# Optimization experiments

Hardware: AMD Instinct MI355X
Metric: run time of the kernel (lower is better)

The kernel has to match this reference:

```python
import jax, jax.numpy as jnp
import numpy as np

B, T, D = 2, 2048, 1024
NH, NKV, HD = 16, 4, 64
BASE, TSL, QGI = 10000.0, 1024, 1.5
EPS = 1.1920929e-07  # torch.finfo(float32).eps used by F.rms_norm default


def _rope_cos_sin(seq_len, rd):
    # Rotary.forward with self.rd == head_dim (Attn sets rd=0 -> full rotation)
    if seq_len > TSL:  # NTK-style base rescale branch
        nb = BASE * (seq_len / TSL) ** (rd / (rd - 2))
    else:
        nb = BASE
    inv = 1.0 / nb ** (jnp.arange(0, rd, 2, dtype=jnp.float32) / rd)
    fr = jnp.arange(seq_len, dtype=jnp.float32)[:, None] * inv[None, :]
    return jnp.cos(fr)[None, :, None, :], jnp.sin(fr)[None, :, None, :]


def _apply_rope(x, cos, sin):
    h = x.shape[-1] // 2
    x1, x2 = x[..., :h], x[..., h:]
    return jnp.concatenate([x1 * cos + x2 * sin, -x1 * sin + x2 * cos], axis=-1)


def _rms_norm(x):
    return x * jax.lax.rsqrt(jnp.mean(x * x, axis=-1, keepdims=True) + EPS)


def setup_inputs() -> dict:
    key = jax.random.key(0)
    ks = jax.random.split(key, 8)
    s = jnp.float32(0.02)
    return {
        "x": jax.random.normal(ks[0], (B, T, D), jnp.float32),
        "qw": jax.random.normal(ks[1], (NH * HD, D), jnp.float32) * s,
        "kw": jax.random.normal(ks[2], (NKV * HD, D), jnp.float32) * s,
        "vw": jax.random.normal(ks[3], (NKV * HD, D), jnp.float32) * s,
        "ow": jax.random.normal(ks[4], (D, D), jnp.float32) * s,
        "ve": jax.random.normal(ks[5], (B, T, NKV * HD), jnp.float32) * s,
        "v0": jax.random.normal(ks[6], (B, T, NKV, HD), jnp.float32) * s,
        "q_gain": jnp.full((NH,), QGI, jnp.float32),
        "vr_lambda": jnp.array([0.5, 0.5], jnp.float32),
        "gate_w": jnp.zeros((NH, D), jnp.float32),      # nn.init.zeros_
        "gate_b": jnp.full((NH,), 4.0, jnp.float32),    # nn.init.constant_(4.0)
    }


def reference(x, qw, kw, vw, ow, ve, v0, q_gain, vr_lambda, gate_w, gate_b):
    # projections
    q = (x @ qw.T).reshape(B, T, NH, HD)
    k = (x @ kw.T).reshape(B, T, NKV, HD)
    v = (x @ vw.T + ve).reshape(B, T, NKV, HD)
    raw_v = v  # returned when vr=True
    v = vr_lambda[0] * v0 + vr_lambda[1] * v  # value residual
    # qk rms-norm + rope (full head dim since self.rd == 0) + per-head q gain
    q = _rms_norm(q)
    k = _rms_norm(k)
    cos, sin = _rope_cos_sin(T, HD)
    q = _apply_rope(q, cos, sin)
    k = _apply_rope(k, cos, sin)
    q = q * q_gain[None, None, :, None]
    # causal GQA attention (nh query heads share nkv kv heads)
    G = NH // NKV
    qg = q.reshape(B, T, NKV, G, HD)
    scale = 1.0 / np.sqrt(HD).astype(np.float32)
    scores = jnp.einsum('bqhgd,bkhd->bhgqk', qg, k) * scale  # [B,NKV,G,T,T]
    causal = jnp.tril(jnp.ones((T, T), bool))
    scores = jnp.where(causal[None, None, None], scores, jnp.finfo(scores.dtype).min)
    p = jax.nn.softmax(scores, axis=-1)
    y = jnp.einsum('bhgqk,bkhd->bqhgd', p, v).reshape(B, T, NH, HD)
    # gated attention output
    gate = jax.nn.sigmoid(x @ gate_w.T + gate_b)  # [B,T,NH]
    y = y * gate[..., None]
    out = y.reshape(B, T, D) @ ow.T
    return out, raw_v
```

## Files before the change

### kernel.cpp

```cpp
#include <hip/hip_runtime.h>
#include <math.h>

#define BB 2
#define TT 2048
#define DD 1024
#define NH 16
#define NKV 4
#define HD 64
#define EPSF 1.1920929e-07f
#define LOG2_NB 14.319970444065578
#define SCALE_LOG2E 0.18033688011112042f
#define FIXMAX 17.5f

typedef __attribute__((ext_vector_type(8))) short bf16x8;
typedef __attribute__((ext_vector_type(4))) float f32x4;

__device__ inline short f2bf(float f) {
    unsigned u = __builtin_bit_cast(unsigned, f);
    unsigned r = (u + 0x7fffu + ((u >> 16) & 1u)) >> 16;
    return (short)r;
}
__device__ inline unsigned cvt_pk_bf16(float a, float b) {
    unsigned r;
    asm("v_cvt_pk_bf16_f32 %0, %1, %2" : "=v"(r) : "v"(a), "v"(b));
    return r;
}

#define GSTAGE(buf, k0, Abase, Bbase)                                                   \
{                                                                                       \
    _Pragma("unroll")                                                                   \
    for (int i_ = 0; i_ < 2; i_++) {                                                    \
        int off = w*2048 + i_*1024;                      \
        int g = (off >> 4) + lane;                                   \
        int row = g >> 2, c = g & 3;                                                    \
        int cg = c ^ (row & 3);                                        \
        const short* ga = (Abase) + (size_t)(m0 + row)*1024 + (k0) + cg*8;              \
        __builtin_amdgcn_global_load_lds(                                               \
            (const __attribute__((address_space(1))) void*)ga,                          \
            (__attribute__((address_space(3))) void*)((char*)&As[buf][0] + off), 16, 0, 0); \
        const short* gb = (Bbase) + (size_t)(n0 + row)*1024 + (k0) + cg*8;              \
        __builtin_amdgcn_global_load_lds(                                               \
            (const __attribute__((address_space(1))) void*)gb,                          \
            (__attribute__((address_space(3))) void*)((char*)&Bs[buf][0] + off), 16, 0, 0); \
    }                                                                                   \
}

#define GEMM_MAIN_LOOP(kbeg, kend, Abase, Bbase)                                        \
    GSTAGE(0, (kbeg), (Abase), (Bbase));                                                \
    __syncthreads();                                                                    \
    for (int k0 = (kbeg); k0 < (kend); k0 += 32) {                                      \
        int cur = ((k0 - (kbeg)) >> 5) & 1;                                             \
        bf16x8 af[4], bfr[4];                                                           \
        _Pragma("unroll")                                                               \
        for (int tm = 0; tm < 4; tm++) {                                                \
            int row = wy*64 + tm*16 + lc;                                               \
            af[tm] = *(const bf16x8*)(&As[cur][0] + row*32 + ((quad*8) ^ ((row&3)*8))); \
        }                                                                               \
        _Pragma("unroll")                                                               \
        for (int tn = 0; tn < 4; tn++) {                                                \
            int row = wx*64 + tn*16 + lc;                                               \
            bfr[tn] = *(const bf16x8*)(&Bs[cur][0] + row*32 + ((quad*8) ^ ((row&3)*8))); \
        }                                                                               \
        if (k0 + 32 < (kend)) GSTAGE(cur ^ 1, k0 + 32, (Abase), (Bbase));               \
        _Pragma("unroll")                                                               \
        for (int tm = 0; tm < 4; tm++)                                                  \
            _Pragma("unroll")                                                           \
            for (int tn = 0; tn < 4; tn++)                                              \
                acc[tm][tn] = __builtin_amdgcn_mfma_f32_16x16x32_bf16(af[tm], bfr[tn], acc[tm][tn], 0, 0, 0); \
        __syncthreads();                                                                \
    }

__global__ __launch_bounds__(256, 2) void gemm_qkv_fused(
    const float* __restrict__ x, const float* __restrict__ qw,
    const float* __restrict__ kw, const float* __restrict__ vw,
    const float* __restrict__ gw, const float* __restrict__ ow,
    const float* __restrict__ ve, const float* __restrict__ v0,
    const float* __restrict__ q_gain, const float* __restrict__ vr_lambda,
    const float* __restrict__ gb_, float* __restrict__ gate,
    short* __restrict__ qbh, short* __restrict__ kbh, short* __restrict__ vtb,
    float* __restrict__ rawv, short* __restrict__ ow16)
{
    __shared__ short As[2][128*32];
    __shared__ short Bs[2][128*32];
    int tid = threadIdx.x;
    int w = tid >> 6, lane = tid & 63;
    int quad = lane >> 4, lc = lane & 15;
    int wy = w >> 1, wx = w & 1;
    int m0 = blockIdx.y * 128, n0 = blockIdx.x * 128;

    int g0 = w*128 + lane;
    int g1 = w*128 + 64 + lane;
    int rA0 = g0 >> 2, rA1 = g1 >> 2;
    int cg0 = (g0 & 3) ^ (rA0 & 3);
    int cg1 = (g1 & 3) ^ (rA1 & 3);
    const float* aptr0 = x + (size_t)(m0 + rA0)*1024 + cg0*8;
    const float* aptr1 = x + (size_t)(m0 + rA1)*1024 + cg1*8;
    int nB0 = n0 + rA0, nB1 = n0 + rA1;
    const float* bptr0;
    if      (nB0 < 1024) bptr0 = qw + (size_t)nB0*1024;
    else if (nB0 < 1280) bptr0 = kw + (size_t)(nB0-1024)*1024;
    else if (nB0 < 1536) bptr0 = vw + (size_t)(nB0-1280)*1024;
    else                 bptr0 = gw + (size_t)((nB0-1536)&15)*1024;
    const float* bptr1;
    if      (nB1 < 1024) bptr1 = qw + (size_t)nB1*1024;
    else if (nB1 < 1280) bptr1 = kw + (size_t)(nB1-1024)*1024;
    else if (nB1 < 1536) bptr1 = vw + (size_t)(nB1-1280)*1024;
    else                 bptr1 = gw + (size_t)((nB1-1536)&15)*1024;
    bptr0 += cg0*8; bptr1 += cg1*8;
    unsigned bmask0 = (nB0 < 1552) ? 0xFFFFFFFFu : 0u;
    unsigned bmask1 = (nB1 < 1552) ? 0xFFFFFFFFu : 0u;

    float4 A0a, A0b, A1a, A1b, B0a, B0b, B1a, B1b;

    #define QSTG_LOAD(k0)                                                   \
    {                                                                       \
        A0a = *(const float4*)(aptr0 + (k0));                               \
        A0b = *(const float4*)(aptr0 + (k0) + 4);                           \
        A1a = *(const float4*)(aptr1 + (k0));                               \
        A1b = *(const float4*)(aptr1 + (k0) + 4);                           \
        B0a = *(const float4*)(bptr0 + (k0));                               \
        B0b = *(const float4*)(bptr0 + (k0) + 4);                           \
        B1a = *(const float4*)(bptr1 + (k0));                               \
        B1b = *(const float4*)(bptr1 + (k0) + 4);                           \
    }

    #define QSTG_WRITE(buf)                                                 \
    {                                                                       \
        unsigned q0, q1, q2, q3; int4 pk;                                   \
        q0 = cvt_pk_bf16(A0a.x, A0a.y); q1 = cvt_pk_bf16(A0a.z, A0a.w);     \
        q2 = cvt_pk_bf16(A0b.x, A0b.y); q3 = cvt_pk_bf16(A0b.z, A0b.w);     \
        pk = (int4){(int)q0,(int)q1,(int)q2,(int)q3};                       \
        *(int4*)((char*)&As[buf][0] + w*2048 + lane*16) = pk;               \
        q0 = cvt_pk_bf16(A1a.x, A1a.y); q1 = cvt_pk_bf16(A1a.z, A1a.w);     \
        q2 = cvt_pk_bf16(A1b.x, A1b.y); q3 = cvt_pk_bf16(A1b.z, A1b.w);     \
        pk = (int4){(int)q0,(int)q1,(int)q2,(int)q3};                       \
        *(int4*)((char*)&As[buf][0] + w*2048 + 1024 + lane*16) = pk;        \
        q0 = cvt_pk_bf16(B0a.x, B0a.y) & bmask0;                            \
        q1 = cvt_pk_bf16(B0a.z, B0a.w) & bmask0;                            \
        q2 = cvt_pk_bf16(B0b.x, B0b.y) & bmask0;                            \
        q3 = cvt_pk_bf16(B0b.z, B0b.w) & bmask0;                            \
        pk = (int4){(int)q0,(int)q1,(int)q2,(int)q3};                       \
        *(int4*)((char*)&Bs[buf][0] + w*2048 + lane*16) = pk;               \
        q0 = cvt_pk_bf16(B1a.x, B1a.y) & bmask1;                            \
        q1 = cvt_pk_bf16(B1a.z, B1a.w) & bmask1;                            \
        q2 = cvt_pk_bf16(B1b.x, B1b.y) & bmask1;                            \
        q3 = cvt_pk_bf16(B1b.z, B1b.w) & bmask1;                            \
        pk = (int4){(int)q0,(int)q1,(int)q2,(int)q3};                       \
        *(int4*)((char*)&Bs[buf][0] + w*2048 + 1024 + lane*16) = pk;        \
    }

    f32x4 acc[4][4];
    #pragma unroll
    for (int i = 0; i < 4; i++)
        #pragma unroll
        for (int j = 0; j < 4; j++) acc[i][j] = (f32x4){0.f,0.f,0.f,0.f};

    QSTG_LOAD(0);
    QSTG_WRITE(0);
    __syncthreads();

    for (int k0 = 0; k0 < 1024; k0 += 32) {
        int cur = (k0 >> 5) & 1;
        bool pre = (k0 + 32) < 1024;
        bf16x8 af[4], bfr[4];
        #pragma unroll
        for (int tm = 0; tm < 4; tm++) {
            int row = wy*64 + tm*16 + lc;
            af[tm] = *(const bf16x8*)(&As[cur][0] + row*32 + ((quad*8) ^ ((row&3)*8)));
        }
        #pragma unroll
        for (int tn = 0; tn < 4; tn++) {
            int row = wx*64 + tn*16 + lc;
            bfr[tn] = *(const bf16x8*)(&Bs[cur][0] + row*32 + ((quad*8) ^ ((row&3)*8)));
        }
        if (pre) QSTG_LOAD(k0 + 32);
        #pragma unroll
        for (int tm = 0; tm < 4; tm++)
            #pragma unroll
            for (int tn = 0; tn < 4; tn++)
                acc[tm][tn] = __builtin_amdgcn_mfma_f32_16x16x32_bf16(af[tm], bfr[tn], acc[tm][tn], 0, 0, 0);
        if (pre) QSTG_WRITE(cur ^ 1);
        __syncthreads();
    }

    int hc = n0 + wx*64;
    if (hc < 1280) {
        bool isq = (hc < 1024);
        int h = isq ? (hc >> 6) : ((hc - 1024) >> 6);
        float gsc = isq ? (q_gain[h] * SCALE_LOG2E) : 1.0f;
        short* dst = isq ? qbh : kbh;
        int nhh = isq ? 16 : 4;
        float inv0 = (float)exp2((double)lc * (-LOG2_NB / 32.0));
        float inv1 = (float)exp2((double)(lc + 16) * (-LOG2_NB / 32.0));
        #pragma unroll
        for (int tm = 0; tm < 4; tm++) {
            #pragma unroll
            for (int r = 0; r < 4; r++) {
                int m = m0 + wy*64 + tm*16 + quad*4 + r;
                int b = m >> 11, t = m & (TT - 1);
                float a0 = acc[tm][0][r], a1 = acc[tm][1][r];
                float a2 = acc[tm][2][r], a3 = acc[tm][3][r];
                float ss = a0*a0 + a1*a1 + a2*a2 + a3*a3;
                ss += __shfl_xor(ss, 1);
                ss += __shfl_xor(ss, 2);
                ss += __shfl_xor(ss, 4);
                ss += __shfl_xor(ss, 8);
                float rn = rsqrtf(ss * (1.0f/64.0f) + EPSF);
                a0 *= rn; a1 *= rn; a2 *= rn; a3 *= rn;
                float sn0, cs0, sn1, cs1;
                sincosf((float)t * inv0, &sn0, &cs0);
                sincosf((float)t * inv1, &sn1, &cs1);
                float o0 = a0*cs0 + a2*sn0;
                float o1 = a1*cs1 + a3*sn1;
                float o2 = a2*cs0 - a0*sn0;
                float o3 = a3*cs1 - a1*sn1;
                size_t base = (((size_t)(b*nhh + h))*2048 + t)*64 + lc;
                dst[base +  0] = f2bf(o0 * gsc);
                dst[base + 16] = f2bf(o1 * gsc);
                dst[base + 32] = f2bf(o2 * gsc);
                dst[base + 48] = f2bf(o3 * gsc);
            }
        }
    } else if (hc < 1536) {
        int kvh = (hc - 1280) >> 6;
        float l0 = vr_lambda[0], l1 = vr_lambda[1];
        short* lbase = (w < 2) ? &As[w][0] : &Bs[w - 2][0];
        #pragma unroll
        for (int tm = 0; tm < 4; tm++) {
            #pragma unroll
            for (int r = 0; r < 4; r++) {
                int m = m0 + wy*64 + tm*16 + quad*4 + r;
                int tl = tm*16 + quad*4 + r;
                size_t off = (size_t)m*256 + kvh*64 + lc;
                #pragma unroll
                for (int tn = 0; tn < 4; tn++) {
                    int d = tn*16 + lc;
                    float val = acc[tm][tn][r] + ve[off + tn*16];
                    rawv[off + tn*16] = val;
                    lbase[d*64 + (tl ^ ((d & 7) * 8))] = f2bf(l0 * v0[off + tn*16] + l1 * val);
                }
            }
        }
        int b = m0 >> 11;
        int t0g = (m0 & 2047) + wy*64;
        short* vdst = vtb + (size_t)(b*4 + kvh)*64*2048;
        #pragma unroll
        for (int j = 0; j < 16; j++) {
            int d = quad + j*4;
            int tc = lc*4;
            short4 vv = *(const short4*)&lbase[d*64 + (tc ^ ((d & 7) * 8))];
            *(short4*)&vdst[(size_t)d*2048 + t0g + tc] = vv;
        }
    } else if (hc == 1536) {
        #pragma unroll
        for (int tm = 0; tm < 4; tm++)
            #pragma unroll
            for (int r = 0; r < 4; r++) {
                int m = m0 + wy*64 + tm*16 + quad*4 + r;
                float lg = acc[tm][0][r] + gb_[lc];
                gate[(size_t)m*16 + lc] = 1.0f / (1.0f + __expf(-lg));
            }
    }

    int gtid = (blockIdx.y * 13 + blockIdx.x) * 256 + tid;
    for (int idx = gtid; idx < 262144; idx += 106496) {
        float4 v = ((const float4*)ow)[idx];
        short4 o;
        o.x = f2bf(v.x); o.y = f2bf(v.y); o.z = f2bf(v.z); o.w = f2bf(v.w);
        ((short4*)ow16)[idx] = o;
    }
    #undef QSTG_LOAD
    #undef QSTG_WRITE
}

__global__ __launch_bounds__(256, 4) void gemm_mfma(
    const short* __restrict__ A, const short* __restrict__ Bmat,
    float* __restrict__ C, int ldc, int klen)
{
    __shared__ short As[2][128*32];
    __shared__ short Bs[2][128*32];
    int tid = threadIdx.x;
    int w = tid >> 6, lane = tid & 63;
    int quad = lane >> 4, lc = lane & 15;
    int wy = w >> 1, wx = w & 1;
    int m0 = blockIdx.y * 128, n0 = blockIdx.x * 128;

    f32x4 acc[4][4];
    #pragma unroll
    for (int i = 0; i < 4; i++)
        #pragma unroll
        for (int j = 0; j < 4; j++) acc[i][j] = (f32x4){0.f,0.f,0.f,0.f};

    GEMM_MAIN_LOOP(0, klen, A, Bmat);

    #pragma unroll
    for (int tm = 0; tm < 4; tm++)
        #pragma unroll
        for (int r = 0; r < 4; r++) {
            int m = m0 + wy*64 + tm*16 + quad*4 + r;
            #pragma unroll
            for (int tn = 0; tn < 4; tn++) {
                int n = n0 + wx*64 + tn*16 + lc;
                C[(size_t)m*ldc + n] = acc[tm][tn][r];
            }
        }
}

__global__ __launch_bounds__(256, 4) void flash_mfma(
    const short* __restrict__ qbh, const short* __restrict__ kbh,
    const short* __restrict__ vtb, const float* __restrict__ gate,
    short* __restrict__ y16)
{
    __shared__ short Ks[2][64*64];
    __shared__ short Vt[2][64*64];
    __shared__ short Ps[4][16*64];

    int bh = blockIdx.x;
    int b = bh >> 4, h = bh & 15, kvh = h >> 2;
    int qt = 31 - blockIdx.y;
    int tid = threadIdx.x;
    int w = tid >> 6, lane = tid & 63;
    int quad = lane >> 4, lc = lane & 15;

    const short* qbase = qbh + (((size_t)bh)*2048 + qt*64 + w*16 + lc)*64;
    bf16x8 qf0 = *(const bf16x8*)(qbase + quad*8);
    bf16x8 qf1 = *(const bf16x8*)(qbase + 32 + quad*8);

    f32x4 o[4];
    #pragma unroll
    for (int i = 0; i < 4; i++) o[i] = (f32x4){0.f,0.f,0.f,0.f};
    f32x4 l4 = (f32x4){0.f,0.f,0.f,0.f};
    const bf16x8 ones = {(short)0x3F80,(short)0x3F80,(short)0x3F80,(short)0x3F80,
                         (short)0x3F80,(short)0x3F80,(short)0x3F80,(short)0x3F80};

    const size_t kbase = ((size_t)(b*4 + kvh))*2048*64;
    const size_t vbase = ((size_t)(b*4 + kvh))*64*2048;

    #define STAGE(buf, kt)                                                              \
    {                                                                                   \
        _Pragma("unroll")                                                               \
        for (int i = 0; i < 2; i++) {                                                   \
            int off = w*2048 + i*1024;                                                  \
            int g = (off >> 4) + lane;                                                  \
            int row = g >> 3, c = g & 7;                                                \
            int cg = c ^ (row & 7);                                                     \
            const short* gk = kbh + kbase + (size_t)((kt)*64 + row)*64 + cg*8;          \
            __builtin_amdgcn_global_load_lds(                                           \
                (const __attribute__((address_space(1))) void*)gk,                      \
                (__attribute__((address_space(3))) void*)((char*)Ks[buf] + off), 16, 0, 0); \
            const short* gv = vtb + vbase + (size_t)row*2048 + (kt)*64 + cg*8;          \
            __builtin_amdgcn_global_load_lds(                                           \
                (const __attribute__((address_space(1))) void*)gv,                      \
                (__attribute__((address_space(3))) void*)((char*)Vt[buf] + off), 16, 0, 0); \
        }                                                                               \
    }

    STAGE(0, 0);
    __syncthreads();

    short* ps = Ps[w];

    for (int kt = 0; kt <= qt; kt++) {
        int cur = kt & 1;
        bool diag = (kt == qt);

        bf16x8 kf0[4], kf1[4], vf0[4], vf1[4];
        #pragma unroll
        for (int kn = 0; kn < 4; kn++) {
            int row = kn*16 + lc;
            int sw = (row & 7) * 8;
            const short* kr = Ks[cur] + row*64;
            kf0[kn] = *(const bf16x8*)(kr + ((quad*8) ^ sw));
            kf1[kn] = *(const bf16x8*)(kr + ((quad*8 + 32) ^ sw));
            const short* vr = Vt[cur] + row*64;
            vf0[kn] = *(const bf16x8*)(vr + ((quad*8) ^ sw));
            vf1[kn] = *(const bf16x8*)(vr + ((quad*8 + 32) ^ sw));
        }
        if (kt < qt) STAGE(cur ^ 1, kt + 1);

        f32x4 s4[4];
        #pragma unroll
        for (int kn = 0; kn < 4; kn++) {
            f32x4 acc = (f32x4){0.f,0.f,0.f,0.f};
            acc = __builtin_amdgcn_mfma_f32_16x16x32_bf16(kf0[kn], qf0, acc, 0, 0, 0);
            acc = __builtin_amdgcn_mfma_f32_16x16x32_bf16(kf1[kn], qf1, acc, 0, 0, 0);
            s4[kn] = acc;
        }

        #pragma unroll
        for (int kn = 0; kn < 4; kn++) {
            float p0 = __builtin_amdgcn_exp2f(s4[kn][0] - FIXMAX);
            float p1 = __builtin_amdgcn_exp2f(s4[kn][1] - FIXMAX);
            float p2 = __builtin_amdgcn_exp2f(s4[kn][2] - FIXMAX);
            float p3 = __builtin_amdgcn_exp2f(s4[kn][3] - FIXMAX);
            if (diag) {
                int keyb = kn*16 + quad*4, qv = w*16 + lc;
                if (keyb + 0 > qv) p0 = 0.f;
                if (keyb + 1 > qv) p1 = 0.f;
                if (keyb + 2 > qv) p2 = 0.f;
                if (keyb + 3 > qv) p3 = 0.f;
            }
            int c = kn*4 + quad;
            int cs = c ^ ((lc & 7) << 1);
            int2 pk;
            pk.x = (int)cvt_pk_bf16(p0, p1);
            pk.y = (int)cvt_pk_bf16(p2, p3);
            *(int2*)(ps + lc*64 + cs*4) = pk;
        }
        __asm__ volatile("s_waitcnt lgkmcnt(0)" ::: "memory");
        int u0 = (0*4 + quad) ^ (lc & 7);
        int u1 = (1*4 + quad) ^ (lc & 7);
        bf16x8 pf0 = *(const bf16x8*)(ps + lc*64 + u0*8);
        bf16x8 pf1 = *(const bf16x8*)(ps + lc*64 + u1*8);

        #pragma unroll
        for (int dn = 0; dn < 4; dn++) {
            o[dn] = __builtin_amdgcn_mfma_f32_16x16x32_bf16(pf0, vf0[dn], o[dn], 0, 0, 0);
            o[dn] = __builtin_amdgcn_mfma_f32_16x16x32_bf16(pf1, vf1[dn], o[dn], 0, 0, 0);
        }
        l4 = __builtin_amdgcn_mfma_f32_16x16x32_bf16(pf0, ones, l4, 0, 0, 0);
        l4 = __builtin_amdgcn_mfma_f32_16x16x32_bf16(pf1, ones, l4, 0, 0, 0);
        __syncthreads();
    }

    #pragma unroll
    for (int r = 0; r < 4; r++) {
        int row = b*2048 + qt*64 + w*16 + quad*4 + r;
        float g = gate[(size_t)row*16 + h] / l4[r];
        #pragma unroll
        for (int dn = 0; dn < 4; dn++)
            y16[(size_t)row*1024 + h*64 + dn*16 + lc] = f2bf(o[dn][r] * g);
    }
}

extern "C" void kernel_launch(void* const* d_in, const int* in_sizes, int n_in,
                              void* d_out, int out_size, void* d_ws, size_t ws_size,
                              hipStream_t stream) {
    (void)in_sizes; (void)n_in; (void)out_size; (void)ws_size;
    const float* x  = (const float*)d_in[0];
    const float* qw = (const float*)d_in[1];
    const float* kw = (const float*)d_in[2];
    const float* vw = (const float*)d_in[3];
    const float* ow = (const float*)d_in[4];
    const float* ve = (const float*)d_in[5];
    const float* v0 = (const float*)d_in[6];
    const float* qg = (const float*)d_in[7];
    const float* vl = (const float*)d_in[8];
    const float* gw = (const float*)d_in[9];
    const float* gb = (const float*)d_in[10];

    float* out  = (float*)d_out;
    float* rawv = out + (size_t)BB*TT*DD;

    float* p    = (float*)d_ws;
    short* ow16 = (short*)p;        p += 524288;
    short* qbh  = (short*)p;        p += 2097152;
    short* kbh  = (short*)p;        p += 524288;
    short* vtb  = (short*)p;        p += 524288;
    float* gt   = p;                p += 65536;
    short* y16  = (short*)p;

    gemm_qkv_fused<<<dim3(13, 32), 256, 0, stream>>>(x, qw, kw, vw, gw, ow,
                                                     ve, v0, qg, vl, gb, gt,
                                                     qbh, kbh, vtb, rawv, ow16);
    flash_mfma<<<dim3(32, 32), 256, 0, stream>>>(qbh, kbh, vtb, gt, y16);
    gemm_mfma<<<dim3(8, 32), 256, 0, stream>>>(y16, ow16, out, 1024, 1024);
}
```

Before: 184.5 us.

## Deepen QKV GEMM global prefetch to two stages and swap grid block order

The fused QKV projection GEMM now keeps two register-staged global loads in flight, unrolling the k loop by two so the next-next tile's fp32 loads are issued while the current tile is being multiplied. The grid is also transposed so consecutive blocks share the same weight column tile and walk over rows of x, which changes L2 reuse of the weight matrices. The deeper prefetch doubles the staging registers, which could raise register pressure under the two-blocks-per-CU launch bound and risk spills.

```diff
diff --git a/kernel.cpp b/kernel.cpp
--- a/kernel.cpp
+++ b/kernel.cpp
@@ -86,7 +86,7 @@
     int w = tid >> 6, lane = tid & 63;
     int quad = lane >> 4, lc = lane & 15;
     int wy = w >> 1, wx = w & 1;
-    int m0 = blockIdx.y * 128, n0 = blockIdx.x * 128;
+    int m0 = blockIdx.x * 128, n0 = blockIdx.y * 128;
 
     int g0 = w*128 + lane;
     int g1 = w*128 + 64 + lane;
@@ -110,44 +110,64 @@
     unsigned bmask0 = (nB0 < 1552) ? 0xFFFFFFFFu : 0u;
     unsigned bmask1 = (nB1 < 1552) ? 0xFFFFFFFFu : 0u;
 
-    float4 A0a, A0b, A1a, A1b, B0a, B0b, B1a, B1b;
-
-    #define QSTG_LOAD(k0)                                                   \
+    float4 A0a0,A0b0,A1a0,A1b0,B0a0,B0b0,B1a0,B1b0;
+    float4 A0a1,A0b1,A1a1,A1b1,B0a1,B0b1,B1a1,B1b1;
+
+    #define QSTG_LOAD(S, k0)                                                \
     {                                                                       \
-        A0a = *(const float4*)(aptr0 + (k0));                               \
-        A0b = *(const float4*)(aptr0 + (k0) + 4);                           \
-        A1a = *(const float4*)(aptr1 + (k0));                               \
-        A1b = *(const float4*)(aptr1 + (k0) + 4);                           \
-        B0a = *(const float4*)(bptr0 + (k0));                               \
-        B0b = *(const float4*)(bptr0 + (k0) + 4);                           \
-        B1a = *(const float4*)(bptr1 + (k0));                               \
-        B1b = *(const float4*)(bptr1 + (k0) + 4);                           \
-    }
-
-    #define QSTG_WRITE(buf)                                                 \
+        A0a##S = *(const float4*)(aptr0 + (k0));                            \
+        A0b##S = *(const float4*)(aptr0 + (k0) + 4);                        \
+        A1a##S = *(const float4*)(aptr1 + (k0));                            \
+        A1b##S = *(const float4*)(aptr1 + (k0) + 4);                        \
+        B0a##S = *(const float4*)(bptr0 + (k0));                            \
+        B0b##S = *(const float4*)(bptr0 + (k0) + 4);                        \
+        B1a##S = *(const float4*)(bptr1 + (k0));                            \
+        B1b##S = *(const float4*)(bptr1 + (k0) + 4);                        \
+    }
+
+    #define QSTG_WRITE(S, buf)                                              \
     {                                                                       \
         unsigned q0, q1, q2, q3; int4 pk;                                   \
-        q0 = cvt_pk_bf16(A0a.x, A0a.y); q1 = cvt_pk_bf16(A0a.z, A0a.w);     \
-        q2 = cvt_pk_bf16(A0b.x, A0b.y); q3 = cvt_pk_bf16(A0b.z, A0b.w);     \
+        q0 = cvt_pk_bf16(A0a##S.x, A0a##S.y); q1 = cvt_pk_bf16(A0a##S.z, A0a##S.w); \
+        q2 = cvt_pk_bf16(A0b##S.x, A0b##S.y); q3 = cvt_pk_bf16(A0b##S.z, A0b##S.w); \
         pk = (int4){(int)q0,(int)q1,(int)q2,(int)q3};                       \
         *(int4*)((char*)&As[buf][0] + w*2048 + lane*16) = pk;               \
-        q0 = cvt_pk_bf16(A1a.x, A1a.y); q1 = cvt_pk_bf16(A1a.z, A1a.w);     \
-        q2 = cvt_pk_bf16(A1b.x, A1b.y); q3 = cvt_pk_bf16(A1b.z, A1b.w);     \
+        q0 = cvt_pk_bf16(A1a##S.x, A1a##S.y); q1 = cvt_pk_bf16(A1a##S.z, A1a##S.w); \
+        q2 = cvt_pk_bf16(A1b##S.x, A1b##S.y); q3 = cvt_pk_bf16(A1b##S.z, A1b##S.w); \
         pk = (int4){(int)q0,(int)q1,(int)q2,(int)q3};                       \
         *(int4*)((char*)&As[buf][0] + w*2048 + 1024 + lane*16) = pk;        \
-        q0 = cvt_pk_bf16(B0a.x, B0a.y) & bmask0;                            \
-        q1 = cvt_pk_bf16(B0a.z, B0a.w) & bmask0;                            \
-        q2 = cvt_pk_bf16(B0b.x, B0b.y) & bmask0;                            \
-        q3 = cvt_pk_bf16(B0b.z, B0b.w) & bmask0;                            \
+        q0 = cvt_pk_bf16(B0a##S.x, B0a##S.y) & bmask0;                      \
+        q1 = cvt_pk_bf16(B0a##S.z, B0a##S.w) & bmask0;                      \
+        q2 = cvt_pk_bf16(B0b##S.x, B0b##S.y) & bmask0;                      \
+        q3 = cvt_pk_bf16(B0b##S.z, B0b##S.w) & bmask0;                      \
         pk = (int4){(int)q0,(int)q1,(int)q2,(int)q3};                       \
         *(int4*)((char*)&Bs[buf][0] + w*2048 + lane*16) = pk;               \
-        q0 = cvt_pk_bf16(B1a.x, B1a.y) & bmask1;                            \
-        q1 = cvt_pk_bf16(B1a.z, B1a.w) & bmask1;                            \
-        q2 = cvt_pk_bf16(B1b.x, B1b.y) & bmask1;                            \
-        q3 = cvt_pk_bf16(B1b.z, B1b.w) & bmask1;                            \
+        q0 = cvt_pk_bf16(B1a##S.x, B1a##S.y) & bmask1;                      \
+        q1 = cvt_pk_bf16(B1a##S.z, B1a##S.w) & bmask1;                      \
+        q2 = cvt_pk_bf16(B1b##S.x, B1b##S.y) & bmask1;                      \
+        q3 = cvt_pk_bf16(B1b##S.z, B1b##S.w) & bmask1;                      \
         pk = (int4){(int)q0,(int)q1,(int)q2,(int)q3};                       \
         *(int4*)((char*)&Bs[buf][0] + w*2048 + 1024 + lane*16) = pk;        \
     }
+
+    #define QFRAGS(buf)                                                     \
+        _Pragma("unroll")                                                   \
+        for (int tm = 0; tm < 4; tm++) {                                    \
+            int row = wy*64 + tm*16 + lc;                                   \
+            af[tm] = *(const bf16x8*)(&As[buf][0] + row*32 + ((quad*8) ^ ((row&3)*8))); \
+        }                                                                   \
+        _Pragma("unroll")                                                   \
+        for (int tn = 0; tn < 4; tn++) {                                    \
+            int row = wx*64 + tn*16 + lc;                                   \
+            bfr[tn] = *(const bf16x8*)(&Bs[buf][0] + row*32 + ((quad*8) ^ ((row&3)*8))); \
+        }
+
+    #define QMFMA                                                           \
+        _Pragma("unroll")                                                   \
+        for (int tm = 0; tm < 4; tm++)                                      \
+            _Pragma("unroll")                                               \
+            for (int tn = 0; tn < 4; tn++)                                  \
+                acc[tm][tn] = __builtin_amdgcn_mfma_f32_16x16x32_bf16(af[tm], bfr[tn], acc[tm][tn], 0, 0, 0);
 
     f32x4 acc[4][4];
     #pragma unroll
@@ -155,31 +175,22 @@
         #pragma unroll
         for (int j = 0; j < 4; j++) acc[i][j] = (f32x4){0.f,0.f,0.f,0.f};
 
-    QSTG_LOAD(0);
-    QSTG_WRITE(0);
+    QSTG_LOAD(0, 0);
+    QSTG_LOAD(1, 32);
+    QSTG_WRITE(0, 0);
     __syncthreads();
 
-    for (int k0 = 0; k0 < 1024; k0 += 32) {
-        int cur = (k0 >> 5) & 1;
-        bool pre = (k0 + 32) < 1024;
+    for (int k0 = 0; k0 < 1024; k0 += 64) {
         bf16x8 af[4], bfr[4];
-        #pragma unroll
-        for (int tm = 0; tm < 4; tm++) {
-            int row = wy*64 + tm*16 + lc;
-            af[tm] = *(const bf16x8*)(&As[cur][0] + row*32 + ((quad*8) ^ ((row&3)*8)));
-        }
-        #pragma unroll
-        for (int tn = 0; tn < 4; tn++) {
-            int row = wx*64 + tn*16 + lc;
-            bfr[tn] = *(const bf16x8*)(&Bs[cur][0] + row*32 + ((quad*8) ^ ((row&3)*8)));
-        }
-        if (pre) QSTG_LOAD(k0 + 32);
-        #pragma unroll
-        for (int tm = 0; tm < 4; tm++)
-            #pragma unroll
-            for (int tn = 0; tn < 4; tn++)
-                acc[tm][tn] = __builtin_amdgcn_mfma_f32_16x16x32_bf16(af[tm], bfr[tn], acc[tm][tn], 0, 0, 0);
-        if (pre) QSTG_WRITE(cur ^ 1);
+        QFRAGS(0);
+        if (k0 + 64 < 1024) QSTG_LOAD(0, k0 + 64);
+        QMFMA;
+        QSTG_WRITE(1, 1);
+        __syncthreads();
+        QFRAGS(1);
+        if (k0 + 96 < 1024) QSTG_LOAD(1, k0 + 96);
+        QMFMA;
+        if (k0 + 64 < 1024) QSTG_WRITE(0, 0);
         __syncthreads();
     }
 
@@ -262,7 +273,7 @@
             }
     }
 
-    int gtid = (blockIdx.y * 13 + blockIdx.x) * 256 + tid;
+    int gtid = (blockIdx.y * 32 + blockIdx.x) * 256 + tid;
     for (int idx = gtid; idx < 262144; idx += 106496) {
         float4 v = ((const float4*)ow)[idx];
         short4 o;
@@ -271,6 +282,8 @@
     }
     #undef QSTG_LOAD
     #undef QSTG_WRITE
+    #undef QFRAGS
+    #undef QMFMA
 }
 
 __global__ __launch_bounds__(256, 4) void gemm_mfma(
@@ -460,7 +473,7 @@
     float* gt   = p;                p += 65536;
     short* y16  = (short*)p;
 
-    gemm_qkv_fused<<<dim3(13, 32), 256, 0, stream>>>(x, qw, kw, vw, gw, ow,
+    gemm_qkv_fused<<<dim3(32, 13), 256, 0, stream>>>(x, qw, kw, vw, gw, ow,
                                                      ve, v0, qg, vl, gb, gt,
                                                      qbh, kbh, vtb, rawv, ow16);
     flash_mfma<<<dim3(32, 32), 256, 0, stream>>>(qbh, kbh, vtb, gt, y16);
```

After: 187.8 us. Within noise of the previous version (+1.8%).
